# Optimization experiments

Measured on AMD Instinct MI355X. Metric: run time of the kernel, lower is better.

The kernel has to match this reference:

```python
import jax, jax.numpy as jnp
import numpy as np

LN2 = 0.6931471805599453

def ssp(x):
    # 'shifted_sp' activation: softplus(x) - log(2)
    return jax.nn.softplus(x) - LN2

def _res_chain(x, W1, b1, W2, b2):
    # PhysNetResidual chain: x <- lin2(ssp(lin1(ssp(x)))) + x
    # W1/W2: [n_res, F, F], b1/b2: [n_res, F]
    for j in range(W1.shape[0]):
        h = ssp(x) @ W1[j] + b1[j]
        x = ssp(h) @ W2[j] + b2[j] + x
    return x

def _physnet_module(feat, radial_aev, idx12, p):
    (W_I, b_I, W_J, b_J, W_gate, gvec, W_int, b_int,
     ri_W1, ri_b1, ri_W2, ri_b2,
     ra_W1, ra_b1, ra_W2, ra_b2,
     ro_W1, ro_b1, ro_W2, ro_b2, W_out, b_out) = p
    N, F = feat.shape
    # self term (no species are dummy -> non_dummy indexing is identity)
    h_self = ssp(ssp(feat) @ W_I + b_I)                       # [N,F]
    # pair messages
    gate = radial_aev @ W_gate                                 # [P,F] (no bias)
    f12 = feat[idx12]                                          # [2,P,F] gather
    fm = ssp(ssp(f12) @ W_J + b_J)                             # [2,P,F]
    pair_msg = gate[None] * fm                                 # [2,P,F]
    proto = jnp.zeros_like(feat).at[idx12.reshape(-1)].add(
        pair_msg.reshape(-1, F))                               # scatter-add
    proto = proto + h_self
    msg = _res_chain(proto, ri_W1, ri_b1, ri_W2, ri_b2)
    feat2 = feat * gvec + ssp(msg) @ W_int + b_int
    feat2 = _res_chain(feat2, ra_W1, ra_b1, ra_W2, ra_b2)
    e = ssp(_res_chain(feat2, ro_W1, ro_b1, ro_W2, ro_b2)) @ W_out + b_out  # [N]
    return e, feat2

def setup_inputs() -> dict:
    key = jax.random.key(0)
    L, F, R = 5, 128, 64
    M, A = 128, 64
    N = M * A
    P = 400000
    ks = jax.random.split(key, 20)
    s = 0.05  # small weight scale keeps activations stable across 5 modules
    inp = {
        'species': jax.random.randint(ks[0], (M, A), 0, 4, dtype=jnp.int32),
        'features': jax.random.normal(ks[1], (N, F), jnp.float32),
        'radial_aev': jax.random.uniform(ks[2], (P, R), jnp.float32),
        'atom_index12': jax.random.randint(ks[3], (2, P), 0, N, dtype=jnp.int32),
        'W_I': jax.random.normal(ks[4], (L, F, F)) * s,
        'b_I': jnp.zeros((L, F)),
        'W_J': jax.random.normal(ks[5], (L, F, F)) * s,
        'b_J': jnp.zeros((L, F)),
        'W_gate': jax.random.normal(ks[6], (L, R, F)) * s,
        'gvec': jnp.ones((L, F)),
        'W_int': jax.random.normal(ks[7], (L, F, F)) * s,
        'b_int': jnp.zeros((L, F)),
        'ri_W1': jax.random.normal(ks[8], (L, 3, F, F)) * s,
        'ri_b1': jnp.zeros((L, 3, F)),
        'ri_W2': jax.random.normal(ks[9], (L, 3, F, F)) * s,
        'ri_b2': jnp.zeros((L, 3, F)),
        'ra_W1': jax.random.normal(ks[10], (L, 2, F, F)) * s,
        'ra_b1': jnp.zeros((L, 2, F)),
        'ra_W2': jax.random.normal(ks[11], (L, 2, F, F)) * s,
        'ra_b2': jnp.zeros((L, 2, F)),
        'ro_W1': jax.random.normal(ks[12], (L, 1, F, F)) * s,
        'ro_b1': jnp.zeros((L, 1, F)),
        'ro_W2': jax.random.normal(ks[13], (L, 1, F, F)) * s,
        'ro_b2': jnp.zeros((L, 1, F)),
        'W_out': jax.random.normal(ks[14], (L, F)) * s,
        'b_out': jnp.zeros((L,)),
    }
    return inp

def reference(species, features, radial_aev, atom_index12,
              W_I, b_I, W_J, b_J, W_gate, gvec, W_int, b_int,
              ri_W1, ri_b1, ri_W2, ri_b2,
              ra_W1, ra_b1, ra_W2, ra_b2,
              ro_W1, ro_b1, ro_W2, ro_b2, W_out, b_out):
    M, A = species.shape
    params = (W_I, b_I, W_J, b_J, W_gate, gvec, W_int, b_int,
              ri_W1, ri_b1, ri_W2, ri_b2,
              ra_W1, ra_b1, ra_W2, ra_b2,
              ro_W1, ro_b1, ro_W2, ro_b2, W_out, b_out)
    feat = features
    energies = jnp.zeros((M * A,), features.dtype)
    for l in range(W_I.shape[0]):  # fixed small module loop
        p = tuple(arr[l] for arr in params)
        e, feat = _physnet_module(feat, radial_aev, atom_index12, p)
        energies = energies + e
    return energies.reshape(M, A), feat
```

## Files before the change

### kernel.cpp

```cpp
#include <hip/hip_runtime.h>


#define LN2F 0.69314718055994530942f
#define NB 128

using short8  = __attribute__((ext_vector_type(8))) short;
using float4v = __attribute__((ext_vector_type(4))) float;
typedef const __attribute__((address_space(1))) unsigned int* gas1_t;
typedef __attribute__((address_space(3))) unsigned int* las3_t;

__device__ __forceinline__ float sspf(float x) {
  float ax = fabsf(x);
  return fmaxf(x, 0.0f) + __logf(1.0f + __expf(-ax)) - LN2F;
}

__device__ __forceinline__ unsigned short f2bf(float x) {
  unsigned int u = __float_as_uint(x);
  u += 0x7fffu + ((u >> 16) & 1u);
  return (unsigned short)(u >> 16);
}

__device__ __forceinline__ void dma16(const void* g, void* l) {
  __builtin_amdgcn_global_load_lds((gas1_t)(unsigned long long)g,
                                   (las3_t)(unsigned long long)l, 16, 0, 0);
}

__device__ __forceinline__ void dma32k(const unsigned short* g, unsigned short* l,
                                       int w, int lane) {
  const char* gb = (const char*)g + w * 4096 + lane * 16;
  char* lb = (char*)l + w * 4096;
#pragma unroll
  for (int i = 0; i < 4; ++i) dma16(gb + i * 1024, lb + i * 1024);
}
__device__ __forceinline__ void dma16k(const unsigned short* g, unsigned short* l,
                                       int w, int lane) {
  const char* gb = (const char*)g + w * 2048 + lane * 16;
  char* lb = (char*)l + w * 2048;
#pragma unroll
  for (int i = 0; i < 2; ++i) dma16(gb + i * 1024, lb + i * 1024);
}

__global__ __launch_bounds__(256) void hist_pass(const int* __restrict__ idx,
                                                 unsigned int* __restrict__ H,
                                                 int n2p, int C) {
  __shared__ unsigned int h[8192];
  int b = blockIdx.x, tid = threadIdx.x;
  for (int i = tid; i < 8192; i += 256) h[i] = 0;
  __syncthreads();
  int s = b * C, e = min(s + C, n2p);
  for (int i = s + tid; i < e; i += 256) atomicAdd(&h[idx[i]], 1u);
  __syncthreads();
  for (int i = tid; i < 8192; i += 256) H[(size_t)b * 8192 + i] = h[i];
}

__global__ __launch_bounds__(256) void col_scan(unsigned int* __restrict__ H,
                                                unsigned int* __restrict__ tot) {
  int a = blockIdx.x * 256 + threadIdx.x;
  unsigned int run = 0;
  for (int b = 0; b < NB; ++b) {
    unsigned int v = H[(size_t)b * 8192 + a];
    H[(size_t)b * 8192 + a] = run;
    run += v;
  }
  tot[a] = run;
}

__global__ __launch_bounds__(256) void scan_kernel(const unsigned int* __restrict__ cnt,
                                                   unsigned int* __restrict__ off, int NA) {
  int t = threadIdx.x;
  unsigned int local[32], s = 0;
#pragma unroll
  for (int i = 0; i < 32; ++i) { local[i] = cnt[t * 32 + i]; s += local[i]; }
  unsigned int v = s;
  int lane = t & 63, w = t >> 6;
#pragma unroll
  for (int o = 1; o < 64; o <<= 1) {
    unsigned int u = __shfl_up(v, o, 64);
    if (lane >= o) v += u;
  }
  __shared__ unsigned int wt4[4];
  if (lane == 63) wt4[w] = v;
  __syncthreads();
  unsigned int base = 0;
  for (int k = 0; k < w; ++k) base += wt4[k];
  unsigned int excl = base + v - s;
#pragma unroll
  for (int i = 0; i < 32; ++i) { off[t * 32 + i] = excl; excl += local[i]; }
  if (t == 255) off[NA] = excl;
}

__global__ __launch_bounds__(256) void place_pass(const int* __restrict__ idx,
                                                  const unsigned int* __restrict__ H,
                                                  const unsigned int* __restrict__ off,
                                                  unsigned int* __restrict__ pairid,
                                                  int P, int C) {
  __shared__ unsigned int pos[8192];
  int b = blockIdx.x, tid = threadIdx.x;
  for (int i = tid; i < 8192; i += 256)
    pos[i] = off[i] + H[(size_t)b * 8192 + i];
  __syncthreads();
  int n2p = 2 * P;
  int s = b * C, e = min(s + C, n2p);
  for (int i = s + tid; i < e; i += 256) {
    int a = idx[i];
    unsigned int p = atomicAdd(&pos[a], 1u);
    pairid[p] = (i >= P) ? (unsigned int)(i - P) : (unsigned int)i;
  }
}

__global__ __launch_bounds__(256) void gather_kernel(const float* __restrict__ radial,
                                                     const unsigned int* __restrict__ off,
                                                     const unsigned int* __restrict__ pairid,
                                                     float* __restrict__ S) {
  __shared__ float red[3][64];
  int a = blockIdx.x;
  int lane = threadIdx.x & 63, w = threadIdx.x >> 6;
  unsigned int b = off[a], e = off[a + 1];
  float acc = 0.0f;
  unsigned int j = b + w;
  while (j + 28 < e) {
    unsigned int p[8];
#pragma unroll
    for (int k = 0; k < 8; ++k) p[k] = pairid[j + 4 * k];
#pragma unroll
    for (int k = 0; k < 8; ++k) acc += radial[(size_t)p[k] * 64 + lane];
    j += 32;
  }
  for (; j < e; j += 4) acc += radial[(size_t)pairid[j] * 64 + lane];
  if (w > 0) red[w - 1][lane] = acc;
  __syncthreads();
  if (w == 0) {
    acc += red[0][lane] + red[1][lane] + red[2][lane];
    S[(size_t)a * 64 + lane] = acc;
  }
}

struct PrepArgs {
  const float* src[80];
  int isgate[80];
};

__global__ __launch_bounds__(256) void prep_weights(PrepArgs A, unsigned short* __restrict__ Wt) {
  int m = blockIdx.x;
  const float* s = A.src[m];
  unsigned short* d = Wt + (size_t)m * 16384;
  if (!A.isgate[m]) {
    for (int it = 0; it < 8; ++it) {
      int q = threadIdx.x + it * 256;
      int n = q & 127, j = q >> 7;
      unsigned short tmp[8];
#pragma unroll
      for (int cc = 0; cc < 8; ++cc) tmp[cc] = f2bf(s[(8 * j + cc) * 128 + n]);
      *(uint4*)(d + (n * 16 + (j ^ (n & 15))) * 8) = *(uint4*)tmp;
    }
  } else {
    for (int it = 0; it < 4; ++it) {
      int q = threadIdx.x + it * 256;
      int n = q & 127, j = q >> 7;
      unsigned short tmp[8];
#pragma unroll
      for (int cc = 0; cc < 8; ++cc) tmp[cc] = f2bf(s[(8 * j + cc) * 128 + n]);
      *(uint4*)(d + (n * 8 + (j ^ (n & 7))) * 8) = *(uint4*)tmp;
    }
  }
}

struct BiasArgs {
  const float* p[17];
  int stride[17];
  const float* b_out;
};

__global__ __launch_bounds__(256) void pack_bias(BiasArgs B, float* __restrict__ dst) {
  int l = blockIdx.x;
  for (int i = threadIdx.x; i < 17 * 128; i += 256) {
    int s = i >> 7;
    dst[(size_t)l * 2304 + i] = B.p[s][l * B.stride[s] + (i & 127)];
  }
  if (threadIdx.x == 0) dst[(size_t)l * 2304 + 17 * 128] = B.b_out[l];
}

struct ChainArgs {
  const float* feat_in;
  const float* S;
  const unsigned short* wt;
  const float* bias_pack;
  float* feat_out;
  float* energy;
};

__device__ __forceinline__ void gemm128s(const unsigned short* sA_, const unsigned short* sW,
                                         int arow, int c, int l16, int quad, float4v acc[2]) {
  const unsigned short* ar = sA_ + (arow + l16) * 136 + quad * 8;
  short8 a0 = *(const short8*)(ar);
  short8 a1 = *(const short8*)(ar + 32);
  short8 a2 = *(const short8*)(ar + 64);
  short8 a3 = *(const short8*)(ar + 96);
#pragma unroll
  for (int f = 0; f < 2; ++f) {
    const unsigned short* bb = sW + (32 * c + 16 * f + l16) * 128;
    acc[f] = __builtin_amdgcn_mfma_f32_16x16x32_bf16(a0, *(const short8*)(bb + ((quad + 0) ^ l16) * 8), acc[f], 0, 0, 0);
    acc[f] = __builtin_amdgcn_mfma_f32_16x16x32_bf16(a1, *(const short8*)(bb + ((quad + 4) ^ l16) * 8), acc[f], 0, 0, 0);
    acc[f] = __builtin_amdgcn_mfma_f32_16x16x32_bf16(a2, *(const short8*)(bb + ((quad + 8) ^ l16) * 8), acc[f], 0, 0, 0);
    acc[f] = __builtin_amdgcn_mfma_f32_16x16x32_bf16(a3, *(const short8*)(bb + ((quad + 12) ^ l16) * 8), acc[f], 0, 0, 0);
  }
}

__device__ __forceinline__ void gemm64s(const unsigned short* sS_, const unsigned short* sW,
                                        int arow, int c, int l16, int quad, float4v acc[2]) {
  const unsigned short* ar = sS_ + (arow + l16) * 72 + quad * 8;
  short8 a0 = *(const short8*)(ar);
  short8 a1 = *(const short8*)(ar + 32);
  int l8 = l16 & 7;
#pragma unroll
  for (int f = 0; f < 2; ++f) {
    const unsigned short* bb = sW + (32 * c + 16 * f + l16) * 64;
    acc[f] = __builtin_amdgcn_mfma_f32_16x16x32_bf16(a0, *(const short8*)(bb + ((quad + 0) ^ l8) * 8), acc[f], 0, 0, 0);
    acc[f] = __builtin_amdgcn_mfma_f32_16x16x32_bf16(a1, *(const short8*)(bb + ((quad + 4) ^ l8) * 8), acc[f], 0, 0, 0);
  }
}

__device__ __forceinline__ void write_ssp_A(unsigned short* sA_, const float4v v[2],
                                            int arow, int c, int l16, int quad) {
#pragma unroll
  for (int f = 0; f < 2; ++f)
#pragma unroll
    for (int r = 0; r < 4; ++r)
      sA_[(arow + quad * 4 + r) * 136 + 32 * c + 16 * f + l16] = f2bf(sspf(v[f][r]));
}

#define Z2(a) { a[0]=Z; a[1]=Z; }

__global__ __launch_bounds__(512) void chain_kernel(ChainArgs A) {
  __shared__ __align__(16) unsigned short swb[2][16384];
  __shared__ __align__(16) unsigned short sA[2][32 * 136];
  __shared__ __align__(16) unsigned short sS[32 * 72];
  __shared__ float sBias[2304];
  __shared__ float sE[32];

  const int tid  = threadIdx.x;
  const int row0 = blockIdx.x * 32;
  const int lane = tid & 63;
  const int w    = tid >> 6;
  const int g    = w >> 2;
  const int c    = w & 3;
  const int l16  = lane & 15;
  const int quad = lane >> 4;
  const int arow = 16 * g;
  const int col0 = 32 * c + l16;

  dma16k(A.wt, swb[0], w, lane);

  for (int i = tid; i < 32 * 64; i += 512) {
    int r = i >> 6, k = i & 63;
    sS[r * 72 + k] = f2bf(A.S[(size_t)(row0 + r) * 64 + k]);
  }
  for (int i = tid; i < 32 * 128; i += 512) {
    int r = i >> 7, k = i & 127;
    sA[0][r * 136 + k] = f2bf(sspf(A.feat_in[(size_t)(row0 + r) * 128 + k]));
  }
  float4v ff[2];
#pragma unroll
  for (int f = 0; f < 2; ++f)
#pragma unroll
    for (int r = 0; r < 4; ++r)
      ff[f][r] = A.feat_in[(size_t)(row0 + arow + quad * 4 + r) * 128 + col0 + 16 * f];
  if (tid < 32) sE[tid] = 0.0f;
  __syncthreads();

  const float4v Z = {0.f, 0.f, 0.f, 0.f};
  float4v gG[2], fm[2], xf[2], t4[2];
  float p0 = 0.f, p1 = 0.f, p2 = 0.f, p3 = 0.f, bsum = 0.f;

#pragma unroll 1
  for (int l = 0; l < 5; ++l) {
    const size_t slot0 = (size_t)l * 16 * 16384;

    dma32k(A.wt + slot0 + 16384, swb[1], w, lane);
    for (int i = tid; i < 2304; i += 512) sBias[i] = A.bias_pack[(size_t)l * 2304 + i];
    Z2(gG);
    gemm64s(sS, swb[0], arow, c, l16, quad, gG);
    __syncthreads();

    dma32k(A.wt + slot0 + 2 * 16384, swb[0], w, lane);
    Z2(fm);
    gemm128s(sA[0], swb[1], arow, c, l16, quad, fm);
#pragma unroll
    for (int f = 0; f < 2; ++f) {
      float bv = sBias[0 * 128 + col0 + 16 * f];
#pragma unroll
      for (int r = 0; r < 4; ++r) fm[f][r] = sspf(fm[f][r] + bv);
    }
    __syncthreads();

    dma32k(A.wt + slot0 + 3 * 16384, swb[1], w, lane);
    Z2(t4);
    gemm128s(sA[0], swb[0], arow, c, l16, quad, t4);
#pragma unroll
    for (int f = 0; f < 2; ++f) {
      float bv = sBias[1 * 128 + col0 + 16 * f];
#pragma unroll
      for (int r = 0; r < 4; ++r) xf[f][r] = fm[f][r] * gG[f][r] + sspf(t4[f][r] + bv);
    }
    write_ssp_A(sA[1], xf, arow, c, l16, quad);
    __syncthreads();

#pragma unroll
    for (int jj = 0; jj < 3; ++jj) {
      const int th = 3 + 2 * jj;
      dma32k(A.wt + slot0 + (size_t)(th + 1) * 16384, swb[th & 1 ? 0 : 1], w, lane);
      Z2(t4);
      gemm128s(sA[1], swb[th & 1], arow, c, l16, quad, t4);
#pragma unroll
      for (int f = 0; f < 2; ++f) {
        float bv = sBias[(th - 1) * 128 + col0 + 16 * f];
#pragma unroll
        for (int r = 0; r < 4; ++r) t4[f][r] += bv;
      }
      write_ssp_A(sA[0], t4, arow, c, l16, quad);
      __syncthreads();

      const int tx = th + 1;
      dma32k(A.wt + slot0 + (size_t)(tx + 1) * 16384, swb[tx & 1 ? 0 : 1], w, lane);
      Z2(t4);
      gemm128s(sA[0], swb[tx & 1], arow, c, l16, quad, t4);
#pragma unroll
      for (int f = 0; f < 2; ++f) {
        float bv = sBias[(tx - 1) * 128 + col0 + 16 * f];
#pragma unroll
        for (int r = 0; r < 4; ++r) xf[f][r] += t4[f][r] + bv;
      }
      write_ssp_A(sA[1], xf, arow, c, l16, quad);
      __syncthreads();
    }

    dma32k(A.wt + slot0 + 10 * 16384, swb[0], w, lane);
    Z2(t4);
    gemm128s(sA[1], swb[1], arow, c, l16, quad, t4);
#pragma unroll
    for (int f = 0; f < 2; ++f) {
      float bv = sBias[8 * 128 + col0 + 16 * f];
      float gv = sBias[15 * 128 + col0 + 16 * f];
#pragma unroll
      for (int r = 0; r < 4; ++r) xf[f][r] = ff[f][r] * gv + t4[f][r] + bv;
    }
    write_ssp_A(sA[0], xf, arow, c, l16, quad);
    __syncthreads();

#pragma unroll
    for (int jj = 0; jj < 2; ++jj) {
      const int th = 10 + 2 * jj;
      dma32k(A.wt + slot0 + (size_t)(th + 1) * 16384, swb[th & 1 ? 0 : 1], w, lane);
      Z2(t4);
      gemm128s(sA[0], swb[th & 1], arow, c, l16, quad, t4);
#pragma unroll
      for (int f = 0; f < 2; ++f) {
        float bv = sBias[(th - 1) * 128 + col0 + 16 * f];
#pragma unroll
        for (int r = 0; r < 4; ++r) t4[f][r] += bv;
      }
      write_ssp_A(sA[1], t4, arow, c, l16, quad);
      __syncthreads();

      const int tx = th + 1;
      dma32k(A.wt + slot0 + (size_t)(tx + 1) * 16384, swb[tx & 1 ? 0 : 1], w, lane);
      Z2(t4);
      gemm128s(sA[1], swb[tx & 1], arow, c, l16, quad, t4);
#pragma unroll
      for (int f = 0; f < 2; ++f) {
        float bv = sBias[(tx - 1) * 128 + col0 + 16 * f];
#pragma unroll
        for (int r = 0; r < 4; ++r) xf[f][r] += t4[f][r] + bv;
      }
      write_ssp_A(sA[0], xf, arow, c, l16, quad);
      __syncthreads();
    }

#pragma unroll
    for (int f = 0; f < 2; ++f) ff[f] = xf[f];
    if (l == 4) {
#pragma unroll
      for (int f = 0; f < 2; ++f)
#pragma unroll
        for (int r = 0; r < 4; ++r)
          A.feat_out[(size_t)(row0 + arow + quad * 4 + r) * 128 + col0 + 16 * f] = xf[f][r];
    }

    dma32k(A.wt + slot0 + 15 * 16384, swb[1], w, lane);
    Z2(t4);
    gemm128s(sA[0], swb[0], arow, c, l16, quad, t4);
#pragma unroll
    for (int f = 0; f < 2; ++f) {
      float bv = sBias[13 * 128 + col0 + 16 * f];
#pragma unroll
      for (int r = 0; r < 4; ++r) t4[f][r] += bv;
    }
    write_ssp_A(sA[1], t4, arow, c, l16, quad);
    __syncthreads();

    if (l < 4) dma16k(A.wt + slot0 + 16 * 16384, swb[0], w, lane);
    Z2(t4);
    gemm128s(sA[1], swb[1], arow, c, l16, quad, t4);
#pragma unroll
    for (int f = 0; f < 2; ++f) {
      float bv = sBias[14 * 128 + col0 + 16 * f];
      float wv = sBias[16 * 128 + col0 + 16 * f];
      p0 += sspf(xf[f][0] + t4[f][0] + bv) * wv;
      p1 += sspf(xf[f][1] + t4[f][1] + bv) * wv;
      p2 += sspf(xf[f][2] + t4[f][2] + bv) * wv;
      p3 += sspf(xf[f][3] + t4[f][3] + bv) * wv;
    }
    bsum += sBias[17 * 128];
    __syncthreads();
  }

#pragma unroll
  for (int o = 1; o < 16; o <<= 1) {
    p0 += __shfl_xor(p0, o, 64);
    p1 += __shfl_xor(p1, o, 64);
    p2 += __shfl_xor(p2, o, 64);
    p3 += __shfl_xor(p3, o, 64);
  }
  if (l16 == 0) {
    atomicAdd(&sE[arow + quad * 4 + 0], p0);
    atomicAdd(&sE[arow + quad * 4 + 1], p1);
    atomicAdd(&sE[arow + quad * 4 + 2], p2);
    atomicAdd(&sE[arow + quad * 4 + 3], p3);
  }
  __syncthreads();
  if (tid < 32) A.energy[row0 + tid] = sE[tid] + bsum;
}

extern "C" void kernel_launch(void* const* d_in, const int* in_sizes, int n_in,
                              void* d_out, int out_size, void* d_ws, size_t ws_size,
                              hipStream_t stream) {
  const float* features = (const float*)d_in[1];
  const float* radial   = (const float*)d_in[2];
  const int*   idx12    = (const int*)  d_in[3];
  const float* W_I    = (const float*)d_in[4];
  const float* b_I    = (const float*)d_in[5];
  const float* W_J    = (const float*)d_in[6];
  const float* b_J    = (const float*)d_in[7];
  const float* W_gate = (const float*)d_in[8];
  const float* gvec   = (const float*)d_in[9];
  const float* W_int  = (const float*)d_in[10];
  const float* b_int  = (const float*)d_in[11];
  const float* ri_W1  = (const float*)d_in[12];
  const float* ri_b1  = (const float*)d_in[13];
  const float* ri_W2  = (const float*)d_in[14];
  const float* ri_b2  = (const float*)d_in[15];
  const float* ra_W1  = (const float*)d_in[16];
  const float* ra_b1  = (const float*)d_in[17];
  const float* ra_W2  = (const float*)d_in[18];
  const float* ra_b2  = (const float*)d_in[19];
  const float* ro_W1  = (const float*)d_in[20];
  const float* ro_b1  = (const float*)d_in[21];
  const float* ro_W2  = (const float*)d_in[22];
  const float* ro_b2  = (const float*)d_in[23];
  const float* W_out  = (const float*)d_in[24];
  const float* b_out  = (const float*)d_in[25];

  const int N = in_sizes[1] / 128;
  const int P = in_sizes[3] / 2;
  const int L = in_sizes[25];
  const int n2p = 2 * P;
  const int C = (n2p + NB - 1) / NB;

  float* S = (float*)d_ws;
  float* bias_pack = S + (size_t)N * 64;
  unsigned short* Wt = (unsigned short*)(bias_pack + 5 * 2304);
  unsigned int* H      = (unsigned int*)(Wt + (size_t)80 * 16384);
  unsigned int* tot    = H + (size_t)NB * 8192;
  unsigned int* off    = tot + N;
  unsigned int* pairid = off + N + 4;

  PrepArgs pa;
  for (int l = 0; l < L; ++l) {
    const float* fx[16] = {
      W_gate + l * 8192,
      W_J + l * 16384, W_I + l * 16384,
      ri_W1 + (l * 3 + 0) * 16384, ri_W2 + (l * 3 + 0) * 16384,
      ri_W1 + (l * 3 + 1) * 16384, ri_W2 + (l * 3 + 1) * 16384,
      ri_W1 + (l * 3 + 2) * 16384, ri_W2 + (l * 3 + 2) * 16384,
      W_int + l * 16384,
      ra_W1 + (l * 2 + 0) * 16384, ra_W2 + (l * 2 + 0) * 16384,
      ra_W1 + (l * 2 + 1) * 16384, ra_W2 + (l * 2 + 1) * 16384,
      ro_W1 + l * 16384, ro_W2 + l * 16384 };
    for (int t = 0; t < 16; ++t) { pa.src[l * 16 + t] = fx[t]; pa.isgate[l * 16 + t] = (t == 0); }
  }
  prep_weights<<<80, 256, 0, stream>>>(pa, Wt);

  BiasArgs ba;
  const float* bp[17] = { b_J, b_I,
    ri_b1, ri_b2, ri_b1 + 128, ri_b2 + 128, ri_b1 + 256, ri_b2 + 256,
    b_int, ra_b1, ra_b2, ra_b1 + 128, ra_b2 + 128, ro_b1, ro_b2, gvec, W_out };
  int st[17] = {128,128, 384,384,384,384,384,384, 128, 256,256,256,256, 128,128,128,128};
  for (int q = 0; q < 17; ++q) { ba.p[q] = bp[q]; ba.stride[q] = st[q]; }
  ba.b_out = b_out;
  pack_bias<<<5, 256, 0, stream>>>(ba, bias_pack);

  hist_pass<<<NB, 256, 0, stream>>>(idx12, H, n2p, C);
  col_scan<<<32, 256, 0, stream>>>(H, tot);
  scan_kernel<<<1, 256, 0, stream>>>(tot, off, N);
  place_pass<<<NB, 256, 0, stream>>>(idx12, H, off, pairid, P, C);
  gather_kernel<<<N, 256, 0, stream>>>(radial, off, pairid, S);

  ChainArgs ca;
  ca.feat_in   = features;
  ca.S         = S;
  ca.wt        = Wt;
  ca.bias_pack = bias_pack;
  ca.energy    = (float*)d_out;
  ca.feat_out  = (float*)d_out + N;
  chain_kernel<<<N / 32, 512, 0, stream>>>(ca);
}
```

Baseline: 369.2 us.

## Double chain kernel wavefronts to 16 per block with one column tile each

The chain kernel now launches 1024 threads per block (16 waves) instead of 512, so each wave computes a single 16x16 output tile instead of two, and the weight-DMA work per wave is halved to match. The gather kernel is rewritten to use predicated batches of 8 loads, so the tail loop is removed and more memory loads stay in flight. Activation bf16 conversion switches to a cheaper round-half-up while weights keep round-to-nearest-even. This trades more barrier participants and per-wave overhead for more latency hiding, and it slightly changes the rounding of activations.

New measurement: 349.5 us. 5.4% less time.

```diff
diff --git a/kernel.cpp b/kernel.cpp
--- a/kernel.cpp
+++ b/kernel.cpp
@@ -15,6 +15,10 @@
 }
 
 __device__ __forceinline__ unsigned short f2bf(float x) {
+  return (unsigned short)((__float_as_uint(x) + 0x8000u) >> 16);
+}
+
+__device__ __forceinline__ unsigned short f2bf_ne(float x) {
   unsigned int u = __float_as_uint(x);
   u += 0x7fffu + ((u >> 16) & 1u);
   return (unsigned short)(u >> 16);
@@ -27,17 +31,14 @@
 
 __device__ __forceinline__ void dma32k(const unsigned short* g, unsigned short* l,
                                        int w, int lane) {
-  const char* gb = (const char*)g + w * 4096 + lane * 16;
-  char* lb = (char*)l + w * 4096;
-#pragma unroll
-  for (int i = 0; i < 4; ++i) dma16(gb + i * 1024, lb + i * 1024);
+  const char* gb = (const char*)g + w * 2048 + lane * 16;
+  char* lb = (char*)l + w * 2048;
+  dma16(gb, lb);
+  dma16(gb + 1024, lb + 1024);
 }
 __device__ __forceinline__ void dma16k(const unsigned short* g, unsigned short* l,
                                        int w, int lane) {
-  const char* gb = (const char*)g + w * 2048 + lane * 16;
-  char* lb = (char*)l + w * 2048;
-#pragma unroll
-  for (int i = 0; i < 2; ++i) dma16(gb + i * 1024, lb + i * 1024);
+  dma16((const char*)g + w * 1024 + lane * 16, (char*)l + w * 1024);
 }
 
 __global__ __launch_bounds__(256) void hist_pass(const int* __restrict__ idx,
@@ -117,16 +118,22 @@
   int lane = threadIdx.x & 63, w = threadIdx.x >> 6;
   unsigned int b = off[a], e = off[a + 1];
   float acc = 0.0f;
-  unsigned int j = b + w;
-  while (j + 28 < e) {
-    unsigned int p[8];
-#pragma unroll
-    for (int k = 0; k < 8; ++k) p[k] = pairid[j + 4 * k];
-#pragma unroll
-    for (int k = 0; k < 8; ++k) acc += radial[(size_t)p[k] * 64 + lane];
-    j += 32;
-  }
-  for (; j < e; j += 4) acc += radial[(size_t)pairid[j] * 64 + lane];
+  for (unsigned int base = b + w; base < e; base += 32) {
+    unsigned int pp[8];
+    float vv[8];
+#pragma unroll
+    for (int k = 0; k < 8; ++k) {
+      unsigned int j = base + 4 * k;
+      pp[k] = pairid[j < e ? j : b];
+    }
+#pragma unroll
+    for (int k = 0; k < 8; ++k) vv[k] = radial[(size_t)pp[k] * 64 + lane];
+#pragma unroll
+    for (int k = 0; k < 8; ++k) {
+      unsigned int j = base + 4 * k;
+      acc += (j < e) ? vv[k] : 0.0f;
+    }
+  }
   if (w > 0) red[w - 1][lane] = acc;
   __syncthreads();
   if (w == 0) {
@@ -150,7 +157,7 @@
       int n = q & 127, j = q >> 7;
       unsigned short tmp[8];
 #pragma unroll
-      for (int cc = 0; cc < 8; ++cc) tmp[cc] = f2bf(s[(8 * j + cc) * 128 + n]);
+      for (int cc = 0; cc < 8; ++cc) tmp[cc] = f2bf_ne(s[(8 * j + cc) * 128 + n]);
       *(uint4*)(d + (n * 16 + (j ^ (n & 15))) * 8) = *(uint4*)tmp;
     }
   } else {
@@ -159,7 +166,7 @@
       int n = q & 127, j = q >> 7;
       unsigned short tmp[8];
 #pragma unroll
-      for (int cc = 0; cc < 8; ++cc) tmp[cc] = f2bf(s[(8 * j + cc) * 128 + n]);
+      for (int cc = 0; cc < 8; ++cc) tmp[cc] = f2bf_ne(s[(8 * j + cc) * 128 + n]);
       *(uint4*)(d + (n * 8 + (j ^ (n & 7))) * 8) = *(uint4*)tmp;
     }
   }
@@ -190,48 +197,38 @@
 };
 
 __device__ __forceinline__ void gemm128s(const unsigned short* sA_, const unsigned short* sW,
-                                         int arow, int c, int l16, int quad, float4v acc[2]) {
+                                         int arow, int col0, int l16, int quad, float4v* acc) {
   const unsigned short* ar = sA_ + (arow + l16) * 136 + quad * 8;
   short8 a0 = *(const short8*)(ar);
   short8 a1 = *(const short8*)(ar + 32);
   short8 a2 = *(const short8*)(ar + 64);
   short8 a3 = *(const short8*)(ar + 96);
-#pragma unroll
-  for (int f = 0; f < 2; ++f) {
-    const unsigned short* bb = sW + (32 * c + 16 * f + l16) * 128;
-    acc[f] = __builtin_amdgcn_mfma_f32_16x16x32_bf16(a0, *(const short8*)(bb + ((quad + 0) ^ l16) * 8), acc[f], 0, 0, 0);
-    acc[f] = __builtin_amdgcn_mfma_f32_16x16x32_bf16(a1, *(const short8*)(bb + ((quad + 4) ^ l16) * 8), acc[f], 0, 0, 0);
-    acc[f] = __builtin_amdgcn_mfma_f32_16x16x32_bf16(a2, *(const short8*)(bb + ((quad + 8) ^ l16) * 8), acc[f], 0, 0, 0);
-    acc[f] = __builtin_amdgcn_mfma_f32_16x16x32_bf16(a3, *(const short8*)(bb + ((quad + 12) ^ l16) * 8), acc[f], 0, 0, 0);
-  }
+  const unsigned short* bb = sW + col0 * 128;
+  *acc = __builtin_amdgcn_mfma_f32_16x16x32_bf16(a0, *(const short8*)(bb + ((quad + 0) ^ l16) * 8), *acc, 0, 0, 0);
+  *acc = __builtin_amdgcn_mfma_f32_16x16x32_bf16(a1, *(const short8*)(bb + ((quad + 4) ^ l16) * 8), *acc, 0, 0, 0);
+  *acc = __builtin_amdgcn_mfma_f32_16x16x32_bf16(a2, *(const short8*)(bb + ((quad + 8) ^ l16) * 8), *acc, 0, 0, 0);
+  *acc = __builtin_amdgcn_mfma_f32_16x16x32_bf16(a3, *(const short8*)(bb + ((quad + 12) ^ l16) * 8), *acc, 0, 0, 0);
 }
 
 __device__ __forceinline__ void gemm64s(const unsigned short* sS_, const unsigned short* sW,
-                                        int arow, int c, int l16, int quad, float4v acc[2]) {
+                                        int arow, int col0, int l16, int quad, float4v* acc) {
   const unsigned short* ar = sS_ + (arow + l16) * 72 + quad * 8;
   short8 a0 = *(const short8*)(ar);
   short8 a1 = *(const short8*)(ar + 32);
   int l8 = l16 & 7;
-#pragma unroll
-  for (int f = 0; f < 2; ++f) {
-    const unsigned short* bb = sW + (32 * c + 16 * f + l16) * 64;
-    acc[f] = __builtin_amdgcn_mfma_f32_16x16x32_bf16(a0, *(const short8*)(bb + ((quad + 0) ^ l8) * 8), acc[f], 0, 0, 0);
-    acc[f] = __builtin_amdgcn_mfma_f32_16x16x32_bf16(a1, *(const short8*)(bb + ((quad + 4) ^ l8) * 8), acc[f], 0, 0, 0);
-  }
-}
-
-__device__ __forceinline__ void write_ssp_A(unsigned short* sA_, const float4v v[2],
-                                            int arow, int c, int l16, int quad) {
-#pragma unroll
-  for (int f = 0; f < 2; ++f)
-#pragma unroll
-    for (int r = 0; r < 4; ++r)
-      sA_[(arow + quad * 4 + r) * 136 + 32 * c + 16 * f + l16] = f2bf(sspf(v[f][r]));
-}
-
-#define Z2(a) { a[0]=Z; a[1]=Z; }
-
-__global__ __launch_bounds__(512) void chain_kernel(ChainArgs A) {
+  const unsigned short* bb = sW + col0 * 64;
+  *acc = __builtin_amdgcn_mfma_f32_16x16x32_bf16(a0, *(const short8*)(bb + ((quad + 0) ^ l8) * 8), *acc, 0, 0, 0);
+  *acc = __builtin_amdgcn_mfma_f32_16x16x32_bf16(a1, *(const short8*)(bb + ((quad + 4) ^ l8) * 8), *acc, 0, 0, 0);
+}
+
+__device__ __forceinline__ void write_ssp_A(unsigned short* sA_, const float4v v,
+                                            int arow, int col0, int quad) {
+#pragma unroll
+  for (int r = 0; r < 4; ++r)
+    sA_[(arow + quad * 4 + r) * 136 + col0] = f2bf(sspf(v[r]));
+}
+
+__global__ __launch_bounds__(1024, 4) void chain_kernel(ChainArgs A) {
   __shared__ __align__(16) unsigned short swb[2][16384];
   __shared__ __align__(16) unsigned short sA[2][32 * 136];
   __shared__ __align__(16) unsigned short sS[32 * 72];
@@ -242,34 +239,32 @@
   const int row0 = blockIdx.x * 32;
   const int lane = tid & 63;
   const int w    = tid >> 6;
-  const int g    = w >> 2;
-  const int c    = w & 3;
+  const int g    = w >> 3;
+  const int c    = w & 7;
   const int l16  = lane & 15;
   const int quad = lane >> 4;
   const int arow = 16 * g;
-  const int col0 = 32 * c + l16;
+  const int col0 = 16 * c + l16;
 
   dma16k(A.wt, swb[0], w, lane);
 
-  for (int i = tid; i < 32 * 64; i += 512) {
+  for (int i = tid; i < 32 * 64; i += 1024) {
     int r = i >> 6, k = i & 63;
     sS[r * 72 + k] = f2bf(A.S[(size_t)(row0 + r) * 64 + k]);
   }
-  for (int i = tid; i < 32 * 128; i += 512) {
+  for (int i = tid; i < 32 * 128; i += 1024) {
     int r = i >> 7, k = i & 127;
     sA[0][r * 136 + k] = f2bf(sspf(A.feat_in[(size_t)(row0 + r) * 128 + k]));
   }
-  float4v ff[2];
-#pragma unroll
-  for (int f = 0; f < 2; ++f)
-#pragma unroll
-    for (int r = 0; r < 4; ++r)
-      ff[f][r] = A.feat_in[(size_t)(row0 + arow + quad * 4 + r) * 128 + col0 + 16 * f];
+  float4v ff;
+#pragma unroll
+  for (int r = 0; r < 4; ++r)
+    ff[r] = A.feat_in[(size_t)(row0 + arow + quad * 4 + r) * 128 + col0];
   if (tid < 32) sE[tid] = 0.0f;
   __syncthreads();
 
   const float4v Z = {0.f, 0.f, 0.f, 0.f};
-  float4v gG[2], fm[2], xf[2], t4[2];
+  float4v gG, fm, xf, t4;
   float p0 = 0.f, p1 = 0.f, p2 = 0.f, p3 = 0.f, bsum = 0.f;
 
 #pragma unroll 1
@@ -277,138 +272,126 @@
     const size_t slot0 = (size_t)l * 16 * 16384;
 
     dma32k(A.wt + slot0 + 16384, swb[1], w, lane);
-    for (int i = tid; i < 2304; i += 512) sBias[i] = A.bias_pack[(size_t)l * 2304 + i];
-    Z2(gG);
-    gemm64s(sS, swb[0], arow, c, l16, quad, gG);
+    for (int i = tid; i < 2304; i += 1024) sBias[i] = A.bias_pack[(size_t)l * 2304 + i];
+    gG = Z;
+    gemm64s(sS, swb[0], arow, col0, l16, quad, &gG);
     __syncthreads();
 
     dma32k(A.wt + slot0 + 2 * 16384, swb[0], w, lane);
-    Z2(fm);
-    gemm128s(sA[0], swb[1], arow, c, l16, quad, fm);
-#pragma unroll
-    for (int f = 0; f < 2; ++f) {
-      float bv = sBias[0 * 128 + col0 + 16 * f];
-#pragma unroll
-      for (int r = 0; r < 4; ++r) fm[f][r] = sspf(fm[f][r] + bv);
+    fm = Z;
+    gemm128s(sA[0], swb[1], arow, col0, l16, quad, &fm);
+    {
+      float bv = sBias[0 * 128 + col0];
+#pragma unroll
+      for (int r = 0; r < 4; ++r) fm[r] = sspf(fm[r] + bv);
     }
     __syncthreads();
 
     dma32k(A.wt + slot0 + 3 * 16384, swb[1], w, lane);
-    Z2(t4);
-    gemm128s(sA[0], swb[0], arow, c, l16, quad, t4);
-#pragma unroll
-    for (int f = 0; f < 2; ++f) {
-      float bv = sBias[1 * 128 + col0 + 16 * f];
-#pragma unroll
-      for (int r = 0; r < 4; ++r) xf[f][r] = fm[f][r] * gG[f][r] + sspf(t4[f][r] + bv);
-    }
-    write_ssp_A(sA[1], xf, arow, c, l16, quad);
+    t4 = Z;
+    gemm128s(sA[0], swb[0], arow, col0, l16, quad, &t4);
+    {
+      float bv = sBias[1 * 128 + col0];
+#pragma unroll
+      for (int r = 0; r < 4; ++r) xf[r] = fm[r] * gG[r] + sspf(t4[r] + bv);
+    }
+    write_ssp_A(sA[1], xf, arow, col0, quad);
     __syncthreads();
 
 #pragma unroll
     for (int jj = 0; jj < 3; ++jj) {
       const int th = 3 + 2 * jj;
       dma32k(A.wt + slot0 + (size_t)(th + 1) * 16384, swb[th & 1 ? 0 : 1], w, lane);
-      Z2(t4);
-      gemm128s(sA[1], swb[th & 1], arow, c, l16, quad, t4);
-#pragma unroll
-      for (int f = 0; f < 2; ++f) {
-        float bv = sBias[(th - 1) * 128 + col0 + 16 * f];
-#pragma unroll
-        for (int r = 0; r < 4; ++r) t4[f][r] += bv;
+      t4 = Z;
+      gemm128s(sA[1], swb[th & 1], arow, col0, l16, quad, &t4);
+      {
+        float bv = sBias[(th - 1) * 128 + col0];
+#pragma unroll
+        for (int r = 0; r < 4; ++r) t4[r] += bv;
       }
-      write_ssp_A(sA[0], t4, arow, c, l16, quad);
+      write_ssp_A(sA[0], t4, arow, col0, quad);
       __syncthreads();
 
       const int tx = th + 1;
       dma32k(A.wt + slot0 + (size_t)(tx + 1) * 16384, swb[tx & 1 ? 0 : 1], w, lane);
-      Z2(t4);
-      gemm128s(sA[0], swb[tx & 1], arow, c, l16, quad, t4);
-#pragma unroll
-      for (int f = 0; f < 2; ++f) {
-        float bv = sBias[(tx - 1) * 128 + col0 + 16 * f];
-#pragma unroll
-        for (int r = 0; r < 4; ++r) xf[f][r] += t4[f][r] + bv;
+      t4 = Z;
+      gemm128s(sA[0], swb[tx & 1], arow, col0, l16, quad, &t4);
+      {
+        float bv = sBias[(tx - 1) * 128 + col0];
+#pragma unroll
+        for (int r = 0; r < 4; ++r) xf[r] += t4[r] + bv;
       }
-      write_ssp_A(sA[1], xf, arow, c, l16, quad);
+      write_ssp_A(sA[1], xf, arow, col0, quad);
       __syncthreads();
     }
 
     dma32k(A.wt + slot0 + 10 * 16384, swb[0], w, lane);
-    Z2(t4);
-    gemm128s(sA[1], swb[1], arow, c, l16, quad, t4);
-#pragma unroll
-    for (int f = 0; f < 2; ++f) {
-      float bv = sBias[8 * 128 + col0 + 16 * f];
-      float gv = sBias[15 * 128 + col0 + 16 * f];
-#pragma unroll
-      for (int r = 0; r < 4; ++r) xf[f][r] = ff[f][r] * gv + t4[f][r] + bv;
-    }
-    write_ssp_A(sA[0], xf, arow, c, l16, quad);
+    t4 = Z;
+    gemm128s(sA[1], swb[1], arow, col0, l16, quad, &t4);
+    {
+      float bv = sBias[8 * 128 + col0];
+      float gv = sBias[15 * 128 + col0];
+#pragma unroll
+      for (int r = 0; r < 4; ++r) xf[r] = ff[r] * gv + t4[r] + bv;
+    }
+    write_ssp_A(sA[0], xf, arow, col0, quad);
     __syncthreads();
 
 #pragma unroll
     for (int jj = 0; jj < 2; ++jj) {
       const int th = 10 + 2 * jj;
       dma32k(A.wt + slot0 + (size_t)(th + 1) * 16384, swb[th & 1 ? 0 : 1], w, lane);
-      Z2(t4);
-      gemm128s(sA[0], swb[th & 1], arow, c, l16, quad, t4);
-#pragma unroll
-      for (int f = 0; f < 2; ++f) {
-        float bv = sBias[(th - 1) * 128 + col0 + 16 * f];
-#pragma unroll
-        for (int r = 0; r < 4; ++r) t4[f][r] += bv;
+      t4 = Z;
+      gemm128s(sA[0], swb[th & 1], arow, col0, l16, quad, &t4);
+      {
+        float bv = sBias[(th - 1) * 128 + col0];
+#pragma unroll
+        for (int r = 0; r < 4; ++r) t4[r] += bv;
       }
-      write_ssp_A(sA[1], t4, arow, c, l16, quad);
+      write_ssp_A(sA[1], t4, arow, col0, quad);
       __syncthreads();
 
       const int tx = th + 1;
       dma32k(A.wt + slot0 + (size_t)(tx + 1) * 16384, swb[tx & 1 ? 0 : 1], w, lane);
-      Z2(t4);
-      gemm128s(sA[1], swb[tx & 1], arow, c, l16, quad, t4);
-#pragma unroll
-      for (int f = 0; f < 2; ++f) {
-        float bv = sBias[(tx - 1) * 128 + col0 + 16 * f];
-#pragma unroll
-        for (int r = 0; r < 4; ++r) xf[f][r] += t4[f][r] + bv;
+      t4 = Z;
+      gemm128s(sA[1], swb[tx & 1], arow, col0, l16, quad, &t4);
+      {
+        float bv = sBias[(tx - 1) * 128 + col0];
+#pragma unroll
+        for (int r = 0; r < 4; ++r) xf[r] += t4[r] + bv;
       }
-      write_ssp_A(sA[0], xf, arow, c, l16, quad);
+      write_ssp_A(sA[0], xf, arow, col0, quad);
       __syncthreads();
     }
 
-#pragma unroll
-    for (int f = 0; f < 2; ++f) ff[f] = xf[f];
+    ff = xf;
     if (l == 4) {
 #pragma unroll
-      for (int f = 0; f < 2; ++f)
-#pragma unroll
-        for (int r = 0; r < 4; ++r)
-          A.feat_out[(size_t)(row0 + arow + quad * 4 + r) * 128 + col0 + 16 * f] = xf[f][r];
+      for (int r = 0; r < 4; ++r)
+        A.feat_out[(size_t)(row0 + arow + quad * 4 + r) * 128 + col0] = xf[r];
     }
 
     dma32k(A.wt + slot0 + 15 * 16384, swb[1], w, lane);
-    Z2(t4);
-    gemm128s(sA[0], swb[0], arow, c, l16, quad, t4);
-#pragma unroll
-    for (int f = 0; f < 2; ++f) {
-      float bv = sBias[13 * 128 + col0 + 16 * f];
-#pragma unroll
-      for (int r = 0; r < 4; ++r) t4[f][r] += bv;
-    }
-    write_ssp_A(sA[1], t4, arow, c, l16, quad);
+    t4 = Z;
+    gemm128s(sA[0], swb[0], arow, col0, l16, quad, &t4);
+    {
+      float bv = sBias[13 * 128 + col0];
+#pragma unroll
+      for (int r = 0; r < 4; ++r) t4[r] += bv;
+    }
+    write_ssp_A(sA[1], t4, arow, col0, quad);
     __syncthreads();
 
     if (l < 4) dma16k(A.wt + slot0 + 16 * 16384, swb[0], w, lane);
-    Z2(t4);
-    gemm128s(sA[1], swb[1], arow, c, l16, quad, t4);
-#pragma unroll
-    for (int f = 0; f < 2; ++f) {
-      float bv = sBias[14 * 128 + col0 + 16 * f];
-      float wv = sBias[16 * 128 + col0 + 16 * f];
-      p0 += sspf(xf[f][0] + t4[f][0] + bv) * wv;
-      p1 += sspf(xf[f][1] + t4[f][1] + bv) * wv;
-      p2 += sspf(xf[f][2] + t4[f][2] + bv) * wv;
-      p3 += sspf(xf[f][3] + t4[f][3] + bv) * wv;
+    t4 = Z;
+    gemm128s(sA[1], swb[1], arow, col0, l16, quad, &t4);
+    {
+      float bv = sBias[14 * 128 + col0];
+      float wv = sBias[16 * 128 + col0];
+      p0 += sspf(xf[0] + t4[0] + bv) * wv;
+      p1 += sspf(xf[1] + t4[1] + bv) * wv;
+      p2 += sspf(xf[2] + t4[2] + bv) * wv;
+      p3 += sspf(xf[3] + t4[3] + bv) * wv;
     }
     bsum += sBias[17 * 128];
     __syncthreads();
@@ -512,5 +495,5 @@
   ca.bias_pack = bias_pack;
   ca.energy    = (float*)d_out;
   ca.feat_out  = (float*)d_out + N;
-  chain_kernel<<<N / 32, 512, 0, stream>>>(ca);
-}
+  chain_kernel<<<N / 32, 1024, 0, stream>>>(ca);
+}
```
